# Performance work log

Measured on AMD Instinct MI355X. Metric: run time of the kernel, lower is better.

## Reference

```python
import jax, jax.numpy as jnp
import numpy as np
from jax import lax

B, N, D_MODEL = 2, 1024, 512
D_INNER, D_STATE, D_CONV, DT_RANK, RED = 1024, 16, 4, 32, 4
EPS = 1e-5


def setup_inputs() -> dict:
    key = jax.random.key(0)
    ks = jax.random.split(key, 40)
    f32 = jnp.float32
    inp = {}
    inp["I1"] = jax.random.normal(ks[0], (B, N, D_MODEL), f32)
    inp["I2"] = jax.random.normal(ks[1], (B, N, D_MODEL), f32)
    inp["norm1_w"] = jnp.ones((D_MODEL,), f32)
    inp["norm1_b"] = jnp.zeros((D_MODEL,), f32)
    inp["norm2_w"] = jnp.ones((D_MODEL,), f32)
    inp["norm2_b"] = jnp.zeros((D_MODEL,), f32)
    inp["se_w1"] = jax.random.normal(ks[2], (D_MODEL // RED, D_MODEL), f32) * 0.02
    inp["se_w2"] = jax.random.normal(ks[3], (D_MODEL, D_MODEL // RED), f32) * 0.02
    A = jnp.tile(jnp.arange(1, D_STATE + 1, dtype=f32), (D_INNER, 1))  # (d_inner, d_state)
    for i, base in ((1, 4), (2, 14)):
        p = f"m{i}_"
        inp[p + "in_w"] = jax.random.normal(ks[base + 0], (2 * D_INNER, D_MODEL), f32) * 0.02
        inp[p + "conv_w"] = jax.random.normal(ks[base + 1], (D_INNER, 1, D_CONV), f32) * 0.1
        inp[p + "conv_b"] = jnp.zeros((D_INNER,), f32)
        inp[p + "xproj_w"] = jax.random.normal(ks[base + 2], (DT_RANK + 2 * D_STATE, D_INNER), f32) * 0.02
        inp[p + "dt_w"] = jax.random.normal(ks[base + 3], (D_INNER, DT_RANK), f32) * 0.02
        inp[p + "dt_b"] = jax.random.normal(ks[base + 4], (D_INNER,), f32) * 0.1
        inp[p + "A_log"] = jnp.log(A)
        inp[p + "D"] = jnp.ones((D_INNER,), f32)
        inp[p + "out_w"] = jax.random.normal(ks[base + 5], (D_MODEL, D_INNER), f32) * 0.02
    return inp


def layernorm(x, w, b):
    mu = x.mean(-1, keepdims=True)
    var = ((x - mu) ** 2).mean(-1, keepdims=True)
    return (x - mu) * lax.rsqrt(var + EPS) * w + b


def silu(x):
    return x * jax.nn.sigmoid(x)


def mamba(x, in_w, conv_w, conv_b, xproj_w, dt_w, dt_b, A_log, Dp, out_w):
    # x: (B, L, d_model)
    b, L, _ = x.shape
    xz = x @ in_w.T                        # (B, L, 2*d_inner)
    xc, z = jnp.split(xz, 2, axis=-1)
    # depthwise causal conv1d over L
    xc = xc.transpose(0, 2, 1)             # (B, d_inner, L)
    xc = jnp.pad(xc, ((0, 0), (0, 0), (D_CONV - 1, 0)))
    xc = lax.conv_general_dilated(xc, conv_w, (1,), "VALID",
                                  dimension_numbers=("NCH", "OIH", "NCH"),
                                  feature_group_count=D_INNER)
    xc = silu(xc + conv_b[None, :, None]).transpose(0, 2, 1)  # (B, L, d_inner)
    x_dbl = xc @ xproj_w.T                 # (B, L, dt_rank + 2*d_state)
    dt, Bm, Cm = jnp.split(x_dbl, [DT_RANK, DT_RANK + D_STATE], axis=-1)
    dt = jax.nn.softplus(dt @ dt_w.T + dt_b)      # (B, L, d_inner)
    A = -jnp.exp(A_log)                           # (d_inner, d_state)
    dA = jnp.exp(dt[..., None] * A)               # (B, L, d_inner, d_state)
    dBu = dt[..., None] * Bm[:, :, None, :] * xc[..., None]

    def step(h, inputs):
        dA_t, dBu_t, C_t = inputs
        h = dA_t * h + dBu_t                      # (B, d_inner, d_state)
        y = jnp.einsum("bds,bs->bd", h, C_t)
        return h, y

    h0 = jnp.zeros((b, D_INNER, D_STATE), x.dtype)
    _, ys = lax.scan(step, h0, (dA.transpose(1, 0, 2, 3),
                                dBu.transpose(1, 0, 2, 3),
                                Cm.transpose(1, 0, 2)))
    y = ys.transpose(1, 0, 2)                     # (B, L, d_inner)
    y = y + xc * Dp
    y = y * silu(z)
    return y @ out_w.T                            # (B, L, d_model)


def se_block(x, w1, w2):
    y = x.mean(axis=1)                            # (B, C)
    y = jax.nn.sigmoid(jax.nn.relu(y @ w1.T) @ w2.T)
    return x * y[:, None, :]


def channel_exchange(x1, x2):
    c = x1.shape[-1]
    mask = (jnp.arange(c) % 2 == 0)               # swap channels where c % p == 0
    return jnp.where(mask, x2, x1), jnp.where(mask, x1, x2)


def reference(I1, I2, norm1_w, norm1_b, norm2_w, norm2_b, se_w1, se_w2,
              m1_in_w, m1_conv_w, m1_conv_b, m1_xproj_w, m1_dt_w, m1_dt_b, m1_A_log, m1_D, m1_out_w,
              m2_in_w, m2_conv_w, m2_conv_b, m2_xproj_w, m2_dt_w, m2_dt_b, m2_A_log, m2_D, m2_out_w):
    I1n = layernorm(I1, norm1_w, norm1_b)
    I2n = layernorm(I2, norm2_w, norm2_b)
    s1, s2 = channel_exchange(I1n, I2n)
    s1 = se_block(s1, se_w1, se_w2)
    s2 = se_block(s2, se_w1, se_w2)
    o1 = mamba(s1, m1_in_w, m1_conv_w, m1_conv_b, m1_xproj_w, m1_dt_w, m1_dt_b, m1_A_log, m1_D, m1_out_w) + I1
    o2 = mamba(s2, m2_in_w, m2_conv_w, m2_conv_b, m2_xproj_w, m2_dt_w, m2_dt_b, m2_A_log, m2_D, m2_out_w) + I2
    return (o1, o2)
```

## Files before the change

### kernel.cpp

```cpp
#include <hip/hip_runtime.h>
#include <hip/hip_bf16.h>

constexpr int kB   = 2;
constexpr int kN   = 1024;
constexpr int kDM  = 512;
constexpr int kDI  = 1024;
constexpr int kDS  = 16;
constexpr int kDTR = 32;
constexpr int kNC  = 32;
constexpr int kCL  = 32;

typedef __attribute__((ext_vector_type(8))) __bf16 bf16x8;
typedef __attribute__((ext_vector_type(4))) __bf16 bf16x4;
typedef __attribute__((ext_vector_type(4))) float  f32x4;

__device__ __forceinline__ float sigmoidf_(float x) { return 1.f / (1.f + __expf(-x)); }
__device__ __forceinline__ float sum4(float4 a) { return a.x + a.y + a.z + a.w; }
__device__ __forceinline__ float dot4(float4 a) { return a.x*a.x + a.y*a.y + a.z*a.z + a.w*a.w; }
__device__ __forceinline__ float4 nrm4(float4 x, float mu, float rs, float4 w, float4 b) {
    return make_float4((x.x-mu)*rs*w.x + b.x, (x.y-mu)*rs*w.y + b.y,
                       (x.z-mu)*rs*w.z + b.z, (x.w-mu)*rs*w.w + b.w);
}
__device__ __forceinline__ bf16x4 tob4(float4 v) {
    return (bf16x4){(__bf16)v.x, (__bf16)v.y, (__bf16)v.z, (__bf16)v.w};
}

__launch_bounds__(256)
__global__ void ln_exchange_k(const float* __restrict__ I1, const float* __restrict__ I2,
                              const float* __restrict__ w1, const float* __restrict__ b1,
                              const float* __restrict__ w2, const float* __restrict__ b2,
                              __bf16* __restrict__ s1b, __bf16* __restrict__ s2b,
                              float* __restrict__ partial)
{
    int w    = threadIdx.x >> 6;
    int row  = blockIdx.x * 4 + w;
    int lane = threadIdx.x & 63;
    const float4* p1 = reinterpret_cast<const float4*>(I1 + (size_t)row * kDM);
    const float4* p2 = reinterpret_cast<const float4*>(I2 + (size_t)row * kDM);
    float4 xa1 = p1[lane], xb1 = p1[lane + 64];
    float4 xa2 = p2[lane], xb2 = p2[lane + 64];
    float su1 = sum4(xa1) + sum4(xb1), sq1 = dot4(xa1) + dot4(xb1);
    float su2 = sum4(xa2) + sum4(xb2), sq2 = dot4(xa2) + dot4(xb2);
    #pragma unroll
    for (int m = 32; m; m >>= 1) {
        su1 += __shfl_xor(su1, m, 64); sq1 += __shfl_xor(sq1, m, 64);
        su2 += __shfl_xor(su2, m, 64); sq2 += __shfl_xor(sq2, m, 64);
    }
    float mu1 = su1 * (1.f / kDM), v1 = sq1 * (1.f / kDM) - mu1 * mu1;
    float mu2 = su2 * (1.f / kDM), v2 = sq2 * (1.f / kDM) - mu2 * mu2;
    float rs1 = rsqrtf(v1 + 1e-5f), rs2 = rsqrtf(v2 + 1e-5f);
    const float4* W1 = reinterpret_cast<const float4*>(w1);
    const float4* B1 = reinterpret_cast<const float4*>(b1);
    const float4* W2 = reinterpret_cast<const float4*>(w2);
    const float4* B2 = reinterpret_cast<const float4*>(b2);
    float4 w1a = W1[lane], w1b = W1[lane+64], b1a = B1[lane], b1b = B1[lane+64];
    float4 w2a = W2[lane], w2b = W2[lane+64], b2a = B2[lane], b2b = B2[lane+64];
    float4 n1a = nrm4(xa1, mu1, rs1, w1a, b1a), n1b = nrm4(xb1, mu1, rs1, w1b, b1b);
    float4 n2a = nrm4(xa2, mu2, rs2, w2a, b2a), n2b = nrm4(xb2, mu2, rs2, w2b, b2b);
    float4 o1a = make_float4(n2a.x, n1a.y, n2a.z, n1a.w);
    float4 o2a = make_float4(n1a.x, n2a.y, n1a.z, n2a.w);
    float4 o1b = make_float4(n2b.x, n1b.y, n2b.z, n1b.w);
    float4 o2b = make_float4(n1b.x, n2b.y, n1b.z, n2b.w);
    bf16x4* q1 = reinterpret_cast<bf16x4*>(s1b + (size_t)row * kDM);
    bf16x4* q2 = reinterpret_cast<bf16x4*>(s2b + (size_t)row * kDM);
    q1[lane] = tob4(o1a); q1[lane + 64] = tob4(o1b);
    q2[lane] = tob4(o2a); q2[lane + 64] = tob4(o2b);

    __shared__ float lp[2][4][kDM];
    int c0 = lane * 4, c1 = 256 + lane * 4;
    lp[0][w][c0+0] = o1a.x; lp[0][w][c0+1] = o1a.y; lp[0][w][c0+2] = o1a.z; lp[0][w][c0+3] = o1a.w;
    lp[0][w][c1+0] = o1b.x; lp[0][w][c1+1] = o1b.y; lp[0][w][c1+2] = o1b.z; lp[0][w][c1+3] = o1b.w;
    lp[1][w][c0+0] = o2a.x; lp[1][w][c0+1] = o2a.y; lp[1][w][c0+2] = o2a.z; lp[1][w][c0+3] = o2a.w;
    lp[1][w][c1+0] = o2b.x; lp[1][w][c1+1] = o2b.y; lp[1][w][c1+2] = o2b.z; lp[1][w][c1+3] = o2b.w;
    __syncthreads();
    for (int c = threadIdx.x; c < kDM; c += 256) {
        partial[((size_t)0 * 512 + blockIdx.x) * kDM + c] =
            lp[0][0][c] + lp[0][1][c] + lp[0][2][c] + lp[0][3][c];
        partial[((size_t)1 * 512 + blockIdx.x) * kDM + c] =
            lp[1][0][c] + lp[1][1][c] + lp[1][2][c] + lp[1][3][c];
    }
}

__launch_bounds__(256)
__global__ void col_red_k(const float* __restrict__ partial, float* __restrict__ partial2)
{
    int x = blockIdx.x;
    int g = x & 31;
    int b = (x >> 5) & 1;
    int t = x >> 6;
    const float* src = partial + ((size_t)t * 512 + b * 256 + g * 8) * kDM;
    float* dst = partial2 + ((size_t)((t * 2 + b) * 32 + g)) * kDM;
    for (int c = threadIdx.x; c < kDM; c += 256) {
        float acc = 0.f;
        #pragma unroll
        for (int i = 0; i < 8; ++i) acc += src[(size_t)i * kDM + c];
        dst[c] = acc;
    }
}

__launch_bounds__(256)
__global__ void se_mlp_k(const float* __restrict__ partial2,
                         const float* __restrict__ w1, const float* __restrict__ w2,
                         float* __restrict__ scl1, float* __restrict__ scl2)
{
    int t = blockIdx.x >> 1, b = blockIdx.x & 1;
    float* scl = (t ? scl2 : scl1) + b * kDM;
    __shared__ float m[kDM];
    __shared__ float hid[128];
    const float* pb = partial2 + (size_t)((t * 2 + b) * 32) * kDM;
    for (int c = threadIdx.x; c < kDM; c += 256) {
        float acc = 0.f;
        #pragma unroll
        for (int i = 0; i < 32; ++i) acc += pb[(size_t)i * kDM + c];
        m[c] = acc * (1.f / kN);
    }
    __syncthreads();
    if (threadIdx.x < 128) {
        int j = threadIdx.x;
        const float4* wv = reinterpret_cast<const float4*>(w1 + (size_t)j * kDM);
        float acc = 0.f;
        #pragma unroll 4
        for (int c = 0; c < kDM; c += 4) {
            float4 w = wv[c >> 2];
            acc = fmaf(m[c+0], w.x, acc);
            acc = fmaf(m[c+1], w.y, acc);
            acc = fmaf(m[c+2], w.z, acc);
            acc = fmaf(m[c+3], w.w, acc);
        }
        hid[j] = fmaxf(acc, 0.f);
    }
    __syncthreads();
    for (int c = threadIdx.x; c < kDM; c += 256) {
        const float4* wv = reinterpret_cast<const float4*>(w2 + (size_t)c * 128);
        float a2 = 0.f;
        #pragma unroll 4
        for (int k = 0; k < 128; k += 4) {
            float4 w = wv[k >> 2];
            a2 = fmaf(hid[k+0], w.x, a2);
            a2 = fmaf(hid[k+1], w.y, a2);
            a2 = fmaf(hid[k+2], w.z, a2);
            a2 = fmaf(hid[k+3], w.w, a2);
        }
        scl[c] = sigmoidf_(a2);
    }
}

__launch_bounds__(256)
__global__ void scale_cvt_all_k(const __bf16* __restrict__ s1b, const __bf16* __restrict__ s2b,
                                const float* __restrict__ scl1, const float* __restrict__ scl2,
                                __bf16* __restrict__ sA0, __bf16* __restrict__ sA1,
                                const float* __restrict__ in0, __bf16* __restrict__ win0,
                                const float* __restrict__ xp0, __bf16* __restrict__ wxp0,
                                const float* __restrict__ ow0, __bf16* __restrict__ wow0,
                                const float* __restrict__ in1, __bf16* __restrict__ win1,
                                const float* __restrict__ xp1, __bf16* __restrict__ wxp1,
                                const float* __restrict__ ow1, __bf16* __restrict__ wow1)
{
    int gidx = blockIdx.x * 256 + threadIdx.x;
    if (gidx < 262144) {
        int mam = gidx >> 17;
        int i = gidx & 131071;
        const __bf16* s = mam ? s2b : s1b;
        const float* scl = mam ? scl2 : scl1;
        __bf16* out = mam ? sA1 : sA0;
        bf16x8 v = reinterpret_cast<const bf16x8*>(s)[i];
        int cg = (i & 63) * 2;
        int row = i >> 6;
        int b = row >> 10;
        const float4* sp = reinterpret_cast<const float4*>(scl + b * kDM);
        float4 sa = sp[cg], sb = sp[cg + 1];
        bf16x8 o;
        o[0] = (__bf16)((float)v[0] * sa.x); o[1] = (__bf16)((float)v[1] * sa.y);
        o[2] = (__bf16)((float)v[2] * sa.z); o[3] = (__bf16)((float)v[3] * sa.w);
        o[4] = (__bf16)((float)v[4] * sb.x); o[5] = (__bf16)((float)v[5] * sb.y);
        o[6] = (__bf16)((float)v[6] * sb.z); o[7] = (__bf16)((float)v[7] * sb.w);
        reinterpret_cast<bf16x8*>(out)[i] = o;
        return;
    }
    int idx = gidx - 262144;
    const float* src; __bf16* dst; int base;
    if (idx < 262144)      { src = in0; dst = win0; base = 0; }
    else if (idx < 278528) { src = xp0; dst = wxp0; base = 262144; }
    else if (idx < 409600) { src = ow0; dst = wow0; base = 278528; }
    else if (idx < 671744) { src = in1; dst = win1; base = 409600; }
    else if (idx < 688128) { src = xp1; dst = wxp1; base = 671744; }
    else                   { src = ow1; dst = wow1; base = 688128; }
    int i = idx - base;
    float4 v = reinterpret_cast<const float4*>(src)[i];
    reinterpret_cast<bf16x4*>(dst)[i] = tob4(v);
}

template<int WM16, int WN16, bool ADD_RES, typename OT>
__global__ __launch_bounds__(256) void gemm_bt2(
    const __bf16* __restrict__ A0, const __bf16* __restrict__ A1,
    const __bf16* __restrict__ B0, const __bf16* __restrict__ B1,
    const float* __restrict__ R0, const float* __restrict__ R1,
    OT* __restrict__ C0, OT* __restrict__ C1,
    int M, int N, int K)
{
    constexpr int WM = 16 * WM16, WN = 16 * WN16;
    int tiles_n = N / WN;
    int tiles_m = M / WM;
    int per = tiles_m * tiles_n;
    int wave = blockIdx.x * (blockDim.x >> 6) + (threadIdx.x >> 6);
    int mam = wave >= per;
    if (mam) wave -= per;
    const __bf16* A  = mam ? A1 : A0;
    const __bf16* Bw = mam ? B1 : B0;
    const float*  R  = mam ? R1 : R0;
    OT*           C  = mam ? C1 : C0;
    int tm = wave / tiles_n, tn = wave % tiles_n;
    int lane = threadIdx.x & 63;
    int r = lane & 15;
    int ko = (lane >> 4) * 8;
    const __bf16* Abase = A  + (size_t)(tm * WM + r) * K + ko;
    const __bf16* Bbase = Bw + (size_t)(tn * WN + r) * K + ko;
    f32x4 acc[WM16][WN16];
    #pragma unroll
    for (int i = 0; i < WM16; ++i)
        #pragma unroll
        for (int j = 0; j < WN16; ++j)
            acc[i][j] = (f32x4){0.f, 0.f, 0.f, 0.f};
    for (int k0 = 0; k0 < K; k0 += 32) {
        bf16x8 a[WM16], b[WN16];
        #pragma unroll
        for (int i = 0; i < WM16; ++i)
            a[i] = *reinterpret_cast<const bf16x8*>(Abase + (size_t)i * 16 * K + k0);
        #pragma unroll
        for (int j = 0; j < WN16; ++j)
            b[j] = *reinterpret_cast<const bf16x8*>(Bbase + (size_t)j * 16 * K + k0);
        #pragma unroll
        for (int i = 0; i < WM16; ++i)
            #pragma unroll
            for (int j = 0; j < WN16; ++j)
                acc[i][j] = __builtin_amdgcn_mfma_f32_16x16x32_bf16(a[i], b[j], acc[i][j], 0, 0, 0);
    }
    int row0 = tm * WM + ((lane >> 4) << 2);
    int col0 = tn * WN + (lane & 15);
    #pragma unroll
    for (int i = 0; i < WM16; ++i)
        #pragma unroll
        for (int j = 0; j < WN16; ++j)
            #pragma unroll
            for (int rr = 0; rr < 4; ++rr) {
                size_t idx = (size_t)(row0 + i * 16 + rr) * N + col0 + j * 16;
                float v = acc[i][j][rr];
                if (ADD_RES) v += R[idx];
                C[idx] = (OT)v;
            }
}

__launch_bounds__(256)
__global__ void conv_silu_k(const __bf16* __restrict__ xz0, const __bf16* __restrict__ xz1,
                            const float* __restrict__ cw0, const float* __restrict__ cw1,
                            const float* __restrict__ cb0, const float* __restrict__ cb1,
                            __bf16* __restrict__ xcb0, __bf16* __restrict__ xcb1)
{
    int gidx = blockIdx.x * 256 + threadIdx.x;
    int mam = gidx >> 21;
    int idx = gidx & ((1 << 21) - 1);
    const __bf16* xz = mam ? xz1 : xz0;
    const float* cw = mam ? cw1 : cw0;
    const float* cb = mam ? cb1 : cb0;
    __bf16* xcb = mam ? xcb1 : xcb0;
    int d = idx & (kDI - 1);
    int n = (idx >> 10) & (kN - 1);
    int b = idx >> 20;
    const __bf16* base = xz + (size_t)(b << 10) * (2 * kDI) + d;
    float acc = cb[d];
    #pragma unroll
    for (int j = 0; j < 4; ++j) {
        int nn = n - 3 + j;
        if (nn >= 0) acc = fmaf((float)base[(size_t)nn * (2 * kDI)], cw[d * 4 + j], acc);
    }
    float o = acc * sigmoidf_(acc);
    xcb[idx] = (__bf16)o;
}

__launch_bounds__(256)
__global__ void dt_softplus_k(const float* __restrict__ xd0, const float* __restrict__ xd1,
                              const float* __restrict__ dtw0, const float* __restrict__ dtw1,
                              const float* __restrict__ dtb0, const float* __restrict__ dtb1,
                              float* __restrict__ out0, float* __restrict__ out1)
{
    int idx = blockIdx.x * 256 + threadIdx.x;
    int d = idx & (kDI - 1);
    int rest = idx >> 10;
    int mblk = rest & 511;
    int mam = rest >> 9;
    const float* xd  = mam ? xd1 : xd0;
    const float* dtw = mam ? dtw1 : dtw0;
    float bias = (mam ? dtb1 : dtb0)[d];
    float* dtout = mam ? out1 : out0;
    float w[kDTR];
    const float4* wv = reinterpret_cast<const float4*>(dtw + (size_t)d * kDTR);
    #pragma unroll
    for (int q = 0; q < 8; ++q) {
        float4 v = wv[q];
        w[q*4+0] = v.x; w[q*4+1] = v.y; w[q*4+2] = v.z; w[q*4+3] = v.w;
    }
    #pragma unroll
    for (int mi = 0; mi < 4; ++mi) {
        int m = mblk * 4 + mi;
        const float4* xv = reinterpret_cast<const float4*>(xd + (size_t)m * 64);
        float acc = bias;
        #pragma unroll
        for (int q = 0; q < 8; ++q) {
            float4 v = xv[q];
            acc = fmaf(v.x, w[q*4+0], acc);
            acc = fmaf(v.y, w[q*4+1], acc);
            acc = fmaf(v.z, w[q*4+2], acc);
            acc = fmaf(v.w, w[q*4+3], acc);
        }
        float sp = acc > 15.f ? acc : log1pf(__expf(acc));
        dtout[(size_t)m * kDI + d] = sp;
    }
}

__device__ __forceinline__ size_t ph_idx(int bm, int c, int s, int d) {
    return (((size_t)bm * kNC + c) * kDS + s) * kDI + d;
}

__launch_bounds__(256)
__global__ void scan_p1(const float* __restrict__ dt_0, const float* __restrict__ dt_1,
                        const __bf16* __restrict__ xc_0, const __bf16* __restrict__ xc_1,
                        const float* __restrict__ xd_0, const float* __restrict__ xd_1,
                        const float* __restrict__ Al_0, const float* __restrict__ Al_1,
                        float* __restrict__ Pbuf, float* __restrict__ Hbuf)
{
    int bid = blockIdx.x;
    int dgrp = bid & 3;
    int c    = (bid >> 2) & (kNC - 1);
    int b    = (bid >> 7) & 1;
    int mam  = bid >> 8;
    int d    = dgrp * 256 + threadIdx.x;
    int bm   = mam * 2 + b;
    const float* dtp = mam ? dt_1 : dt_0;
    const __bf16* xcp = mam ? xc_1 : xc_0;
    const float* xdp = mam ? xd_1 : xd_0;
    const float* Alp = mam ? Al_1 : Al_0;

    float a[kDS], h[kDS], P[kDS];
    {
        const float4* Av = reinterpret_cast<const float4*>(Alp + d * kDS);
        #pragma unroll
        for (int q = 0; q < 4; ++q) {
            float4 v = Av[q];
            a[q*4+0] = -__expf(v.x); a[q*4+1] = -__expf(v.y);
            a[q*4+2] = -__expf(v.z); a[q*4+3] = -__expf(v.w);
        }
    }
    #pragma unroll
    for (int s = 0; s < kDS; ++s) { h[s] = 0.f; P[s] = 1.f; }

    int t0 = c * kCL;
    const float* dtr = dtp + ((size_t)b * kN + t0) * kDI + d;
    const __bf16* xcr = xcp + ((size_t)b * kN + t0) * kDI + d;
    const float4* xdr = reinterpret_cast<const float4*>(xdp + ((size_t)b * kN + t0) * 64);

    #pragma unroll 4
    for (int t = 0; t < kCL; ++t) {
        float dtv = dtr[(size_t)t * kDI];
        float xcv = (float)xcr[(size_t)t * kDI];
        float4 B0 = xdr[t * 16 + 8],  B1 = xdr[t * 16 + 9];
        float4 B2 = xdr[t * 16 + 10], B3 = xdr[t * 16 + 11];
        float Bv[kDS] = {B0.x,B0.y,B0.z,B0.w, B1.x,B1.y,B1.z,B1.w,
                         B2.x,B2.y,B2.z,B2.w, B3.x,B3.y,B3.z,B3.w};
        float dtxc = dtv * xcv;
        #pragma unroll
        for (int s = 0; s < kDS; ++s) {
            float dA = __expf(dtv * a[s]);
            P[s] *= dA;
            h[s] = fmaf(dA, h[s], dtxc * Bv[s]);
        }
    }
    #pragma unroll
    for (int s = 0; s < kDS; ++s) {
        Pbuf[ph_idx(bm, c, s, d)] = P[s];
        Hbuf[ph_idx(bm, c, s, d)] = h[s];
    }
}

__launch_bounds__(256)
__global__ void scan_p2(const float* __restrict__ Pbuf, const float* __restrict__ Hbuf,
                        float* __restrict__ Init)
{
    int i = blockIdx.x * 256 + threadIdx.x;
    int d = i & (kDI - 1);
    int s = (i >> 10) & 15;
    int bm = i >> 14;
    float h = 0.f;
    #pragma unroll 4
    for (int c = 0; c < kNC; ++c) {
        size_t o = ph_idx(bm, c, s, d);
        Init[o] = h;
        h = fmaf(Pbuf[o], h, Hbuf[o]);
    }
}

__launch_bounds__(256)
__global__ void scan_p3(const float* __restrict__ dt_0, const float* __restrict__ dt_1,
                        const __bf16* __restrict__ xc_0, const __bf16* __restrict__ xc_1,
                        const __bf16* __restrict__ xz_0, const __bf16* __restrict__ xz_1,
                        const float* __restrict__ xd_0, const float* __restrict__ xd_1,
                        const float* __restrict__ Al_0, const float* __restrict__ Al_1,
                        const float* __restrict__ Dp_0, const float* __restrict__ Dp_1,
                        const float* __restrict__ Init,
                        __bf16* __restrict__ yg_0, __bf16* __restrict__ yg_1)
{
    int bid = blockIdx.x;
    int dgrp = bid & 3;
    int c    = (bid >> 2) & (kNC - 1);
    int b    = (bid >> 7) & 1;
    int mam  = bid >> 8;
    int d    = dgrp * 256 + threadIdx.x;
    int bm   = mam * 2 + b;
    const float* dtp = mam ? dt_1 : dt_0;
    const __bf16* xcp = mam ? xc_1 : xc_0;
    const __bf16* xzp = mam ? xz_1 : xz_0;
    const float* xdp = mam ? xd_1 : xd_0;
    const float* Alp = mam ? Al_1 : Al_0;
    const float* Dpp = mam ? Dp_1 : Dp_0;
    __bf16* ygp = mam ? yg_1 : yg_0;

    float a[kDS], h[kDS];
    {
        const float4* Av = reinterpret_cast<const float4*>(Alp + d * kDS);
        #pragma unroll
        for (int q = 0; q < 4; ++q) {
            float4 v = Av[q];
            a[q*4+0] = -__expf(v.x); a[q*4+1] = -__expf(v.y);
            a[q*4+2] = -__expf(v.z); a[q*4+3] = -__expf(v.w);
        }
    }
    #pragma unroll
    for (int s = 0; s < kDS; ++s) h[s] = Init[ph_idx(bm, c, s, d)];
    float Dd = Dpp[d];

    int t0 = c * kCL;
    const float* dtr = dtp + ((size_t)b * kN + t0) * kDI + d;
    const __bf16* xcr = xcp + ((size_t)b * kN + t0) * kDI + d;
    const __bf16* zr  = xzp + ((size_t)b * kN + t0) * 2 * kDI + kDI + d;
    const float4* xdr = reinterpret_cast<const float4*>(xdp + ((size_t)b * kN + t0) * 64);
    __bf16* yr = ygp + ((size_t)b * kN + t0) * kDI + d;

    #pragma unroll 4
    for (int t = 0; t < kCL; ++t) {
        float dtv = dtr[(size_t)t * kDI];
        float xcv = (float)xcr[(size_t)t * kDI];
        float zv  = (float)zr[(size_t)t * 2 * kDI];
        float4 B0 = xdr[t * 16 + 8],  B1 = xdr[t * 16 + 9];
        float4 B2 = xdr[t * 16 + 10], B3 = xdr[t * 16 + 11];
        float4 C0 = xdr[t * 16 + 12], C1 = xdr[t * 16 + 13];
        float4 C2 = xdr[t * 16 + 14], C3 = xdr[t * 16 + 15];
        float Bv[kDS] = {B0.x,B0.y,B0.z,B0.w, B1.x,B1.y,B1.z,B1.w,
                         B2.x,B2.y,B2.z,B2.w, B3.x,B3.y,B3.z,B3.w};
        float Cv[kDS] = {C0.x,C0.y,C0.z,C0.w, C1.x,C1.y,C1.z,C1.w,
                         C2.x,C2.y,C2.z,C2.w, C3.x,C3.y,C3.z,C3.w};
        float dtxc = dtv * xcv;
        float acc0 = 0.f, acc1 = 0.f, acc2 = 0.f, acc3 = 0.f;
        #pragma unroll
        for (int s = 0; s < kDS; s += 4) {
            float dA0 = __expf(dtv * a[s+0]);
            float dA1 = __expf(dtv * a[s+1]);
            float dA2 = __expf(dtv * a[s+2]);
            float dA3 = __expf(dtv * a[s+3]);
            h[s+0] = fmaf(dA0, h[s+0], dtxc * Bv[s+0]);
            h[s+1] = fmaf(dA1, h[s+1], dtxc * Bv[s+1]);
            h[s+2] = fmaf(dA2, h[s+2], dtxc * Bv[s+2]);
            h[s+3] = fmaf(dA3, h[s+3], dtxc * Bv[s+3]);
            acc0 = fmaf(h[s+0], Cv[s+0], acc0);
            acc1 = fmaf(h[s+1], Cv[s+1], acc1);
            acc2 = fmaf(h[s+2], Cv[s+2], acc2);
            acc3 = fmaf(h[s+3], Cv[s+3], acc3);
        }
        float y = (acc0 + acc1) + (acc2 + acc3) + xcv * Dd;
        yr[(size_t)t * kDI] = (__bf16)(y * zv * sigmoidf_(zv));
    }
}

extern "C" void kernel_launch(void* const* d_in, const int* in_sizes, int n_in,
                              void* d_out, int out_size, void* d_ws, size_t ws_size,
                              hipStream_t stream)
{
    (void)in_sizes; (void)n_in; (void)out_size; (void)ws_size;
    const float* I1  = (const float*)d_in[0];
    const float* I2  = (const float*)d_in[1];
    const float* n1w = (const float*)d_in[2];
    const float* n1b = (const float*)d_in[3];
    const float* n2w = (const float*)d_in[4];
    const float* n2b = (const float*)d_in[5];
    const float* sew1 = (const float*)d_in[6];
    const float* sew2 = (const float*)d_in[7];
    const float* in_w[2]   = {(const float*)d_in[8],  (const float*)d_in[17]};
    const float* conv_w[2] = {(const float*)d_in[9],  (const float*)d_in[18]};
    const float* conv_b[2] = {(const float*)d_in[10], (const float*)d_in[19]};
    const float* xp_w[2]   = {(const float*)d_in[11], (const float*)d_in[20]};
    const float* dt_w[2]   = {(const float*)d_in[12], (const float*)d_in[21]};
    const float* dt_b[2]   = {(const float*)d_in[13], (const float*)d_in[22]};
    const float* A_log[2]  = {(const float*)d_in[14], (const float*)d_in[23]};
    const float* Dp[2]     = {(const float*)d_in[15], (const float*)d_in[24]};
    const float* out_w[2]  = {(const float*)d_in[16], (const float*)d_in[25]};

    char* base = (char*)d_ws;
    size_t off = 0;
    auto alloc = [&](size_t bytes) -> char* {
        char* p = base + off;
        off = (off + bytes + 255) & ~(size_t)255;
        return p;
    };
    __bf16*  s1b  = (__bf16*)alloc((size_t)2 << 20);
    __bf16*  s2b  = (__bf16*)alloc((size_t)2 << 20);
    float*   partial  = (float*)alloc((size_t)2 * 512 * kDM * 4);
    float*   partial2 = (float*)alloc((size_t)128 * kDM * 4);
    float*   scl1 = (float*)alloc(1024 * 4);
    float*   scl2 = (float*)alloc(1024 * 4);
    __bf16*  sA[2]    = {(__bf16*)alloc((size_t)2 << 20), (__bf16*)alloc((size_t)2 << 20)};
    __bf16*  w_in[2]  = {(__bf16*)alloc((size_t)2 << 20), (__bf16*)alloc((size_t)2 << 20)};
    __bf16*  w_xp[2]  = {(__bf16*)alloc((size_t)128 << 10), (__bf16*)alloc((size_t)128 << 10)};
    __bf16*  w_out[2] = {(__bf16*)alloc((size_t)1 << 20), (__bf16*)alloc((size_t)1 << 20)};
    __bf16*  xzb[2] = {(__bf16*)alloc((size_t)8 << 20), (__bf16*)alloc((size_t)8 << 20)};
    __bf16*  xcb[2] = {(__bf16*)alloc((size_t)4 << 20), (__bf16*)alloc((size_t)4 << 20)};
    float*   xd[2]  = {(float*)alloc((size_t)512 << 10), (float*)alloc((size_t)512 << 10)};
    float*   dts[2] = {(float*)alloc((size_t)8 << 20),  (float*)alloc((size_t)8 << 20)};
    __bf16*  yg[2]  = {(__bf16*)alloc((size_t)4 << 20), (__bf16*)alloc((size_t)4 << 20)};
    float*   Pbuf   = (float*)alloc((size_t)8 << 20);
    float*   Hbuf   = (float*)alloc((size_t)8 << 20);
    float*   Init   = (float*)alloc((size_t)8 << 20);
    float* o1 = (float*)d_out;
    float* o2 = o1 + (size_t)kB * kN * kDM;

    ln_exchange_k<<<512, 256, 0, stream>>>(I1, I2, n1w, n1b, n2w, n2b, s1b, s2b, partial);
    col_red_k<<<128, 256, 0, stream>>>(partial, partial2);
    se_mlp_k<<<4, 256, 0, stream>>>(partial2, sew1, sew2, scl1, scl2);
    scale_cvt_all_k<<<4224, 256, 0, stream>>>(s1b, s2b, scl1, scl2, sA[0], sA[1],
                                              in_w[0], w_in[0], xp_w[0], w_xp[0],
                                              out_w[0], w_out[0],
                                              in_w[1], w_in[1], xp_w[1], w_xp[1],
                                              out_w[1], w_out[1]);
    gemm_bt2<4, 8, false, __bf16><<<256, 256, 0, stream>>>(
        sA[0], sA[1], w_in[0], w_in[1], nullptr, nullptr, xzb[0], xzb[1],
        kB * kN, 2 * kDI, kDM);
    conv_silu_k<<<16384, 256, 0, stream>>>(xzb[0], xzb[1], conv_w[0], conv_w[1],
                                           conv_b[0], conv_b[1], xcb[0], xcb[1]);
    gemm_bt2<1, 2, false, float><<<128, 256, 0, stream>>>(
        xcb[0], xcb[1], w_xp[0], w_xp[1], nullptr, nullptr, xd[0], xd[1],
        kB * kN, 64, kDI);
    dt_softplus_k<<<4096, 256, 0, stream>>>(xd[0], xd[1], dt_w[0], dt_w[1],
                                            dt_b[0], dt_b[1], dts[0], dts[1]);
    scan_p1<<<512, 256, 0, stream>>>(dts[0], dts[1], xcb[0], xcb[1], xd[0], xd[1],
                                     A_log[0], A_log[1], Pbuf, Hbuf);
    scan_p2<<<256, 256, 0, stream>>>(Pbuf, Hbuf, Init);
    scan_p3<<<512, 256, 0, stream>>>(dts[0], dts[1], xcb[0], xcb[1], xzb[0], xzb[1],
                                     xd[0], xd[1], A_log[0], A_log[1], Dp[0], Dp[1],
                                     Init, yg[0], yg[1]);
    gemm_bt2<2, 4, true, float><<<256, 256, 0, stream>>>(
        yg[0], yg[1], w_out[0], w_out[1], I1, I2, o1, o2, kB * kN, kDM, kDI);
}
```

Before: 214.0 us.

## Fuse dt projection into scan, bf16 scan buffers, LDS-staged in-proj GEMM

Result: faster. 206.0 us (-3.7%).

```diff
diff --git a/kernel.cpp b/kernel.cpp
--- a/kernel.cpp
+++ b/kernel.cpp
@@ -13,6 +13,10 @@
 typedef __attribute__((ext_vector_type(8))) __bf16 bf16x8;
 typedef __attribute__((ext_vector_type(4))) __bf16 bf16x4;
 typedef __attribute__((ext_vector_type(4))) float  f32x4;
+
+#define GLD16(g, l) __builtin_amdgcn_global_load_lds( \
+    (const __attribute__((address_space(1))) void*)(g), \
+    (__attribute__((address_space(3))) void*)(l), 16, 0, 0)
 
 __device__ __forceinline__ float sigmoidf_(float x) { return 1.f / (1.f + __expf(-x)); }
 __device__ __forceinline__ float sum4(float4 a) { return a.x + a.y + a.z + a.w; }
@@ -190,6 +194,76 @@
     reinterpret_cast<bf16x4*>(dst)[i] = tob4(v);
 }
 
+template<typename OT>
+__global__ __launch_bounds__(256) void gemm_lds_k(
+    const __bf16* __restrict__ A0, const __bf16* __restrict__ A1,
+    const __bf16* __restrict__ B0, const __bf16* __restrict__ B1,
+    OT* __restrict__ C0, OT* __restrict__ C1,
+    int M, int N, int K)
+{
+    __shared__ __bf16 lA[128 * 32];
+    __shared__ __bf16 lB[128 * 32];
+    int tiles_n = N >> 7, tiles_m = M >> 7;
+    int per = tiles_m * tiles_n;
+    int blk = blockIdx.x;
+    int mam = blk >= per;
+    if (mam) blk -= per;
+    const __bf16* A  = mam ? A1 : A0;
+    const __bf16* Bw = mam ? B1 : B0;
+    OT*           C  = mam ? C1 : C0;
+    int tm = blk / tiles_n, tn = blk % tiles_n;
+    int tid = threadIdx.x;
+    int w = tid >> 6, lane = tid & 63;
+    int wr = w >> 1, wc = w & 1;
+
+    f32x4 acc[4][4];
+    #pragma unroll
+    for (int i = 0; i < 4; ++i)
+        #pragma unroll
+        for (int j = 0; j < 4; ++j)
+            acc[i][j] = (f32x4){0.f, 0.f, 0.f, 0.f};
+
+    const __bf16* Abase = A  + (size_t)tm * 128 * K;
+    const __bf16* Bbase = Bw + (size_t)tn * 128 * K;
+    int srow = (lane >> 2);
+    int skk  = (lane & 3) * 8;
+
+    for (int k0 = 0; k0 < K; k0 += 32) {
+        #pragma unroll
+        for (int r = 0; r < 2; ++r) {
+            int seg = r * 4 + w;
+            int row = seg * 16 + srow;
+            GLD16(Abase + (size_t)row * K + k0 + skk, &lA[seg * 512]);
+            GLD16(Bbase + (size_t)row * K + k0 + skk, &lB[seg * 512]);
+        }
+        __syncthreads();
+        bf16x8 af[4], bfr[4];
+        #pragma unroll
+        for (int i = 0; i < 4; ++i)
+            af[i] = *reinterpret_cast<const bf16x8*>(
+                &lA[(wr * 64 + i * 16 + (lane & 15)) * 32 + (lane >> 4) * 8]);
+        #pragma unroll
+        for (int j = 0; j < 4; ++j)
+            bfr[j] = *reinterpret_cast<const bf16x8*>(
+                &lB[(wc * 64 + j * 16 + (lane & 15)) * 32 + (lane >> 4) * 8]);
+        #pragma unroll
+        for (int i = 0; i < 4; ++i)
+            #pragma unroll
+            for (int j = 0; j < 4; ++j)
+                acc[i][j] = __builtin_amdgcn_mfma_f32_16x16x32_bf16(af[i], bfr[j], acc[i][j], 0, 0, 0);
+        __syncthreads();
+    }
+    int row0 = tm * 128 + wr * 64 + ((lane >> 4) << 2);
+    int col0 = tn * 128 + wc * 64 + (lane & 15);
+    #pragma unroll
+    for (int i = 0; i < 4; ++i)
+        #pragma unroll
+        for (int j = 0; j < 4; ++j)
+            #pragma unroll
+            for (int rr = 0; rr < 4; ++rr)
+                C[(size_t)(row0 + i * 16 + rr) * N + col0 + j * 16] = (OT)acc[i][j][rr];
+}
+
 template<int WM16, int WN16, bool ADD_RES, typename OT>
 __global__ __launch_bounds__(256) void gemm_bt2(
     const __bf16* __restrict__ A0, const __bf16* __restrict__ A1,
@@ -277,56 +351,32 @@
     xcb[idx] = (__bf16)o;
 }
 
-__launch_bounds__(256)
-__global__ void dt_softplus_k(const float* __restrict__ xd0, const float* __restrict__ xd1,
-                              const float* __restrict__ dtw0, const float* __restrict__ dtw1,
-                              const float* __restrict__ dtb0, const float* __restrict__ dtb1,
-                              float* __restrict__ out0, float* __restrict__ out1)
-{
-    int idx = blockIdx.x * 256 + threadIdx.x;
-    int d = idx & (kDI - 1);
-    int rest = idx >> 10;
-    int mblk = rest & 511;
-    int mam = rest >> 9;
-    const float* xd  = mam ? xd1 : xd0;
-    const float* dtw = mam ? dtw1 : dtw0;
-    float bias = (mam ? dtb1 : dtb0)[d];
-    float* dtout = mam ? out1 : out0;
-    float w[kDTR];
-    const float4* wv = reinterpret_cast<const float4*>(dtw + (size_t)d * kDTR);
-    #pragma unroll
-    for (int q = 0; q < 8; ++q) {
-        float4 v = wv[q];
-        w[q*4+0] = v.x; w[q*4+1] = v.y; w[q*4+2] = v.z; w[q*4+3] = v.w;
-    }
-    #pragma unroll
-    for (int mi = 0; mi < 4; ++mi) {
-        int m = mblk * 4 + mi;
-        const float4* xv = reinterpret_cast<const float4*>(xd + (size_t)m * 64);
-        float acc = bias;
-        #pragma unroll
-        for (int q = 0; q < 8; ++q) {
-            float4 v = xv[q];
-            acc = fmaf(v.x, w[q*4+0], acc);
-            acc = fmaf(v.y, w[q*4+1], acc);
-            acc = fmaf(v.z, w[q*4+2], acc);
-            acc = fmaf(v.w, w[q*4+3], acc);
-        }
-        float sp = acc > 15.f ? acc : log1pf(__expf(acc));
-        dtout[(size_t)m * kDI + d] = sp;
-    }
-}
-
 __device__ __forceinline__ size_t ph_idx(int bm, int c, int s, int d) {
     return (((size_t)bm * kNC + c) * kDS + s) * kDI + d;
 }
 
-__launch_bounds__(256)
-__global__ void scan_p1(const float* __restrict__ dt_0, const float* __restrict__ dt_1,
-                        const __bf16* __restrict__ xc_0, const __bf16* __restrict__ xc_1,
+__device__ __forceinline__ float dt_inline(const float4* __restrict__ xdr, int t,
+                                           const float* __restrict__ wdt, float bias)
+{
+    float acc = bias;
+    #pragma unroll
+    for (int q = 0; q < 8; ++q) {
+        float4 v = xdr[t * 16 + q];
+        acc = fmaf(v.x, wdt[q*4+0], acc);
+        acc = fmaf(v.y, wdt[q*4+1], acc);
+        acc = fmaf(v.z, wdt[q*4+2], acc);
+        acc = fmaf(v.w, wdt[q*4+3], acc);
+    }
+    return acc > 15.f ? acc : log1pf(__expf(acc));
+}
+
+__launch_bounds__(256)
+__global__ void scan_p1(const __bf16* __restrict__ xc_0, const __bf16* __restrict__ xc_1,
                         const float* __restrict__ xd_0, const float* __restrict__ xd_1,
+                        const float* __restrict__ dtw0, const float* __restrict__ dtw1,
+                        const float* __restrict__ dtb0, const float* __restrict__ dtb1,
                         const float* __restrict__ Al_0, const float* __restrict__ Al_1,
-                        float* __restrict__ Pbuf, float* __restrict__ Hbuf)
+                        __bf16* __restrict__ Pbuf, __bf16* __restrict__ Hbuf)
 {
     int bid = blockIdx.x;
     int dgrp = bid & 3;
@@ -335,11 +385,21 @@
     int mam  = bid >> 8;
     int d    = dgrp * 256 + threadIdx.x;
     int bm   = mam * 2 + b;
-    const float* dtp = mam ? dt_1 : dt_0;
     const __bf16* xcp = mam ? xc_1 : xc_0;
     const float* xdp = mam ? xd_1 : xd_0;
     const float* Alp = mam ? Al_1 : Al_0;
-
+    const float* dtw = mam ? dtw1 : dtw0;
+    float bias = (mam ? dtb1 : dtb0)[d];
+
+    float wdt[kDTR];
+    {
+        const float4* wv = reinterpret_cast<const float4*>(dtw + (size_t)d * kDTR);
+        #pragma unroll
+        for (int q = 0; q < 8; ++q) {
+            float4 v = wv[q];
+            wdt[q*4+0] = v.x; wdt[q*4+1] = v.y; wdt[q*4+2] = v.z; wdt[q*4+3] = v.w;
+        }
+    }
     float a[kDS], h[kDS], P[kDS];
     {
         const float4* Av = reinterpret_cast<const float4*>(Alp + d * kDS);
@@ -354,13 +414,11 @@
     for (int s = 0; s < kDS; ++s) { h[s] = 0.f; P[s] = 1.f; }
 
     int t0 = c * kCL;
-    const float* dtr = dtp + ((size_t)b * kN + t0) * kDI + d;
     const __bf16* xcr = xcp + ((size_t)b * kN + t0) * kDI + d;
     const float4* xdr = reinterpret_cast<const float4*>(xdp + ((size_t)b * kN + t0) * 64);
 
-    #pragma unroll 4
     for (int t = 0; t < kCL; ++t) {
-        float dtv = dtr[(size_t)t * kDI];
+        float dtv = dt_inline(xdr, t, wdt, bias);
         float xcv = (float)xcr[(size_t)t * kDI];
         float4 B0 = xdr[t * 16 + 8],  B1 = xdr[t * 16 + 9];
         float4 B2 = xdr[t * 16 + 10], B3 = xdr[t * 16 + 11];
@@ -376,14 +434,14 @@
     }
     #pragma unroll
     for (int s = 0; s < kDS; ++s) {
-        Pbuf[ph_idx(bm, c, s, d)] = P[s];
-        Hbuf[ph_idx(bm, c, s, d)] = h[s];
-    }
-}
-
-__launch_bounds__(256)
-__global__ void scan_p2(const float* __restrict__ Pbuf, const float* __restrict__ Hbuf,
-                        float* __restrict__ Init)
+        Pbuf[ph_idx(bm, c, s, d)] = (__bf16)P[s];
+        Hbuf[ph_idx(bm, c, s, d)] = (__bf16)h[s];
+    }
+}
+
+__launch_bounds__(256)
+__global__ void scan_p2(const __bf16* __restrict__ Pbuf, const __bf16* __restrict__ Hbuf,
+                        __bf16* __restrict__ Init)
 {
     int i = blockIdx.x * 256 + threadIdx.x;
     int d = i & (kDI - 1);
@@ -393,19 +451,20 @@
     #pragma unroll 4
     for (int c = 0; c < kNC; ++c) {
         size_t o = ph_idx(bm, c, s, d);
-        Init[o] = h;
-        h = fmaf(Pbuf[o], h, Hbuf[o]);
-    }
-}
-
-__launch_bounds__(256)
-__global__ void scan_p3(const float* __restrict__ dt_0, const float* __restrict__ dt_1,
-                        const __bf16* __restrict__ xc_0, const __bf16* __restrict__ xc_1,
+        Init[o] = (__bf16)h;
+        h = fmaf((float)Pbuf[o], h, (float)Hbuf[o]);
+    }
+}
+
+__launch_bounds__(256)
+__global__ void scan_p3(const __bf16* __restrict__ xc_0, const __bf16* __restrict__ xc_1,
                         const __bf16* __restrict__ xz_0, const __bf16* __restrict__ xz_1,
                         const float* __restrict__ xd_0, const float* __restrict__ xd_1,
+                        const float* __restrict__ dtw0, const float* __restrict__ dtw1,
+                        const float* __restrict__ dtb0, const float* __restrict__ dtb1,
                         const float* __restrict__ Al_0, const float* __restrict__ Al_1,
                         const float* __restrict__ Dp_0, const float* __restrict__ Dp_1,
-                        const float* __restrict__ Init,
+                        const __bf16* __restrict__ Init,
                         __bf16* __restrict__ yg_0, __bf16* __restrict__ yg_1)
 {
     int bid = blockIdx.x;
@@ -415,14 +474,24 @@
     int mam  = bid >> 8;
     int d    = dgrp * 256 + threadIdx.x;
     int bm   = mam * 2 + b;
-    const float* dtp = mam ? dt_1 : dt_0;
     const __bf16* xcp = mam ? xc_1 : xc_0;
     const __bf16* xzp = mam ? xz_1 : xz_0;
     const float* xdp = mam ? xd_1 : xd_0;
     const float* Alp = mam ? Al_1 : Al_0;
     const float* Dpp = mam ? Dp_1 : Dp_0;
+    const float* dtw = mam ? dtw1 : dtw0;
+    float bias = (mam ? dtb1 : dtb0)[d];
     __bf16* ygp = mam ? yg_1 : yg_0;
 
+    float wdt[kDTR];
+    {
+        const float4* wv = reinterpret_cast<const float4*>(dtw + (size_t)d * kDTR);
+        #pragma unroll
+        for (int q = 0; q < 8; ++q) {
+            float4 v = wv[q];
+            wdt[q*4+0] = v.x; wdt[q*4+1] = v.y; wdt[q*4+2] = v.z; wdt[q*4+3] = v.w;
+        }
+    }
     float a[kDS], h[kDS];
     {
         const float4* Av = reinterpret_cast<const float4*>(Alp + d * kDS);
@@ -434,19 +503,17 @@
         }
     }
     #pragma unroll
-    for (int s = 0; s < kDS; ++s) h[s] = Init[ph_idx(bm, c, s, d)];
+    for (int s = 0; s < kDS; ++s) h[s] = (float)Init[ph_idx(bm, c, s, d)];
     float Dd = Dpp[d];
 
     int t0 = c * kCL;
-    const float* dtr = dtp + ((size_t)b * kN + t0) * kDI + d;
     const __bf16* xcr = xcp + ((size_t)b * kN + t0) * kDI + d;
     const __bf16* zr  = xzp + ((size_t)b * kN + t0) * 2 * kDI + kDI + d;
     const float4* xdr = reinterpret_cast<const float4*>(xdp + ((size_t)b * kN + t0) * 64);
     __bf16* yr = ygp + ((size_t)b * kN + t0) * kDI + d;
 
-    #pragma unroll 4
     for (int t = 0; t < kCL; ++t) {
-        float dtv = dtr[(size_t)t * kDI];
+        float dtv = dt_inline(xdr, t, wdt, bias);
         float xcv = (float)xcr[(size_t)t * kDI];
         float zv  = (float)zr[(size_t)t * 2 * kDI];
         float4 B0 = xdr[t * 16 + 8],  B1 = xdr[t * 16 + 9];
@@ -522,11 +589,10 @@
     __bf16*  xzb[2] = {(__bf16*)alloc((size_t)8 << 20), (__bf16*)alloc((size_t)8 << 20)};
     __bf16*  xcb[2] = {(__bf16*)alloc((size_t)4 << 20), (__bf16*)alloc((size_t)4 << 20)};
     float*   xd[2]  = {(float*)alloc((size_t)512 << 10), (float*)alloc((size_t)512 << 10)};
-    float*   dts[2] = {(float*)alloc((size_t)8 << 20),  (float*)alloc((size_t)8 << 20)};
     __bf16*  yg[2]  = {(__bf16*)alloc((size_t)4 << 20), (__bf16*)alloc((size_t)4 << 20)};
-    float*   Pbuf   = (float*)alloc((size_t)8 << 20);
-    float*   Hbuf   = (float*)alloc((size_t)8 << 20);
-    float*   Init   = (float*)alloc((size_t)8 << 20);
+    __bf16*  Pbuf   = (__bf16*)alloc((size_t)4 << 20);
+    __bf16*  Hbuf   = (__bf16*)alloc((size_t)4 << 20);
+    __bf16*  Init   = (__bf16*)alloc((size_t)4 << 20);
     float* o1 = (float*)d_out;
     float* o2 = o1 + (size_t)kB * kN * kDM;
 
@@ -538,22 +604,21 @@
                                               out_w[0], w_out[0],
                                               in_w[1], w_in[1], xp_w[1], w_xp[1],
                                               out_w[1], w_out[1]);
-    gemm_bt2<4, 8, false, __bf16><<<256, 256, 0, stream>>>(
-        sA[0], sA[1], w_in[0], w_in[1], nullptr, nullptr, xzb[0], xzb[1],
-        kB * kN, 2 * kDI, kDM);
+    gemm_lds_k<__bf16><<<512, 256, 0, stream>>>(
+        sA[0], sA[1], w_in[0], w_in[1], xzb[0], xzb[1], kB * kN, 2 * kDI, kDM);
     conv_silu_k<<<16384, 256, 0, stream>>>(xzb[0], xzb[1], conv_w[0], conv_w[1],
                                            conv_b[0], conv_b[1], xcb[0], xcb[1]);
     gemm_bt2<1, 2, false, float><<<128, 256, 0, stream>>>(
         xcb[0], xcb[1], w_xp[0], w_xp[1], nullptr, nullptr, xd[0], xd[1],
         kB * kN, 64, kDI);
-    dt_softplus_k<<<4096, 256, 0, stream>>>(xd[0], xd[1], dt_w[0], dt_w[1],
-                                            dt_b[0], dt_b[1], dts[0], dts[1]);
-    scan_p1<<<512, 256, 0, stream>>>(dts[0], dts[1], xcb[0], xcb[1], xd[0], xd[1],
+    scan_p1<<<512, 256, 0, stream>>>(xcb[0], xcb[1], xd[0], xd[1],
+                                     dt_w[0], dt_w[1], dt_b[0], dt_b[1],
                                      A_log[0], A_log[1], Pbuf, Hbuf);
     scan_p2<<<256, 256, 0, stream>>>(Pbuf, Hbuf, Init);
-    scan_p3<<<512, 256, 0, stream>>>(dts[0], dts[1], xcb[0], xcb[1], xzb[0], xzb[1],
-                                     xd[0], xd[1], A_log[0], A_log[1], Dp[0], Dp[1],
+    scan_p3<<<512, 256, 0, stream>>>(xcb[0], xcb[1], xzb[0], xzb[1], xd[0], xd[1],
+                                     dt_w[0], dt_w[1], dt_b[0], dt_b[1],
+                                     A_log[0], A_log[1], Dp[0], Dp[1],
                                      Init, yg[0], yg[1]);
-    gemm_bt2<2, 4, true, float><<<256, 256, 0, stream>>>(
+    gemm_bt2<2, 2, true, float><<<512, 256, 0, stream>>>(
         yg[0], yg[1], w_out[0], w_out[1], I1, I2, o1, o2, kB * kN, kDM, kDI);
 }
```
